# Optimization experiments

Hardware: AMD Instinct MI355X
Metric: run time of the kernel (lower is better)

## Reference

```python
import jax, jax.numpy as jnp
import numpy as np
from math import factorial, comb

N_NODES = 50000
N_EDGES = 640000
FEAT = 32
NUM_BASIS = 8
CUTOFF = 5.0
MAX_Z = 118
NUM_ITERS = 3
LMAX = 2
K = (LMAX + 1) ** 2  # 9 spherical channels for max_degree=2


def _assoc_legendre(c, s, lmax):
    # associated Legendre P_l^m without Condon-Shortley phase
    P = {(0, 0): np.ones_like(c)}
    for m in range(1, lmax + 1):
        P[(m, m)] = P[(m - 1, m - 1)] * (2 * m - 1) * s
    for m in range(lmax):
        P[(m + 1, m)] = (2 * m + 1) * c * P[(m, m)]
    for m in range(lmax + 1):
        for l in range(m + 2, lmax + 1):
            P[(l, m)] = ((2 * l - 1) * c * P[(l - 1, m)] - (l + m - 1) * P[(l - 2, m)]) / (l - m)
    return P


def _real_sh_np(xyz, lmax):
    # Racah-normalized real spherical harmonics (Y_00 = 1), order m=-l..l
    r = np.linalg.norm(xyz, axis=1)
    cth = xyz[:, 2] / r
    sth = np.sqrt(np.maximum(1.0 - cth ** 2, 0.0))
    phi = np.arctan2(xyz[:, 1], xyz[:, 0])
    P = _assoc_legendre(cth, sth, lmax)
    cols = []
    for l in range(lmax + 1):
        for m in range(-l, l + 1):
            am = abs(m)
            if m == 0:
                cols.append(P[(l, 0)])
            else:
                nrm = np.sqrt(2.0 * factorial(l - am) / factorial(l + am))
                ang = np.cos(am * phi) if m > 0 else np.sin(am * phi)
                cols.append(nrm * P[(l, am)] * ang)
    return np.stack(cols, axis=1)


def _gaunt_tensor():
    # cg[k1,k2,k3]: expansion of Y_k1 * Y_k2 onto Y_k3 (degrees <= 2).
    # Products of degree<=2 harmonics lie exactly in span of degree<=4 harmonics,
    # so the least-squares fit below recovers exact coefficients.
    rng = np.random.default_rng(0)
    pts = rng.normal(size=(4096, 3))
    pts /= np.linalg.norm(pts, axis=1, keepdims=True)
    A = _real_sh_np(pts, 2 * LMAX)  # (M, 25)
    Y = A[:, :K]                    # (M, 9)
    prod = (Y[:, :, None] * Y[:, None, :]).reshape(len(pts), K * K)
    coef, *_ = np.linalg.lstsq(A, prod, rcond=None)  # (25, 81)
    return coef[:K].reshape(K, K, K).transpose(1, 2, 0).astype(np.float32)


CG = jnp.asarray(_gaunt_tensor())  # (9, 9, 9)
LOG_BINOM = jnp.asarray([np.log(comb(NUM_BASIS - 1, kk)) for kk in range(NUM_BASIS)], dtype=jnp.float32)


def _sh_l2(u):
    # Racah real SH of unit vectors, degrees 0..2, order m=-l..l
    x, y, z = u[:, 0], u[:, 1], u[:, 2]
    s3 = 1.7320508075688772
    return jnp.stack([
        jnp.ones_like(x),
        y, z, x,
        s3 * x * y, s3 * y * z, 0.5 * (3.0 * z * z - 1.0), s3 * x * z, 0.5 * s3 * (x * x - y * y),
    ], axis=1)


def _radial(r):
    # reciprocal Bernstein basis (log-space, stable) * smooth cutoff
    u = r / (1.0 + r)
    k = jnp.arange(NUM_BASIS, dtype=jnp.float32)
    n = float(NUM_BASIS - 1)
    eps = 1e-12
    logu = jnp.log(jnp.maximum(u, eps))[:, None]
    log1u = jnp.log(jnp.maximum(1.0 - u, eps))[:, None]
    bern = jnp.exp(LOG_BINOM + k * logu + (n - k) * log1u)  # (E, B)
    cut = jnp.where(r < CUTOFF, jnp.exp(-(r * r) / jnp.maximum(CUTOFF * CUTOFF - r * r, eps)), 0.0)
    return bern * cut[:, None]


def _forward(dr_vec, embed, rad_w, d1w, d1b, d2w, d2b, Z, neighbor_idxs):
    idx_i, idx_j = neighbor_idxs[0], neighbor_idxs[1]
    r = jnp.linalg.norm(dr_vec, axis=1)
    u = dr_vec / jnp.maximum(r, 1e-9)[:, None]
    Ysh = _sh_l2(u)              # (E, 9) angular basis
    rad = _radial(r)             # (E, B) radial basis
    # mask padding edges (idx_i == idx_j) as in mask_by_neighbor
    rad = rad * (idx_i != idx_j).astype(rad.dtype)[:, None]

    N = Z.shape[0]
    x = jnp.zeros((N, K, FEAT), jnp.float32).at[:, 0, :].set(embed[Z])

    for i in range(NUM_ITERS):
        last = i == NUM_ITERS - 1
        k3 = 1 if last else K    # last MessagePass has max_degree=0
        xe = x[idx_j]                                  # (E, 9, F) edge gather
        g = jnp.einsum('eb,dbf->edf', rad, rad_w[i])   # (E, 3, F) radial->feature per basis degree
        y = jnp.zeros((N_EDGES, k3, FEAT), jnp.float32)
        for l2 in range(LMAX + 1):
            sl = slice(l2 * l2, (l2 + 1) ** 2)
            c = jnp.einsum('abc,eb->eac', CG[:, sl, :k3], Ysh[:, sl])          # (E, 9, k3)
            y = y + jnp.einsum('eac,eaf->ecf', c, xe * g[:, l2][:, None, :])   # (E, k3, F)
        m = jax.ops.segment_sum(y, idx_i, num_segments=N)                      # scatter-sum
        if last:
            x = x[:, :1, :]      # change_max_degree_or_type(x, 0)
        h = x + m
        h = jnp.einsum('nkf,fg->nkg', h, d1w[i]).at[:, 0, :].add(d1b[i])
        gate = jax.nn.sigmoid(h[:, :1, :])
        h = h * gate             # silu on scalar channel, sigmoid-gated tensor channels
        h = jnp.einsum('nkf,fg->nkg', h, d2w[i]).at[:, 0, :].add(d2b[i])
        x = x + h
    return x[:, 0, :]            # (N, F)


def setup_inputs() -> dict:
    key = jax.random.key(0)
    ks = jax.random.split(key, 8)
    dr_vec = jax.random.normal(ks[0], (N_EDGES, 3), jnp.float32) * 2.0
    Z = jax.random.randint(ks[1], (N_NODES,), 0, MAX_Z + 1, jnp.int32)
    neighbor_idxs = jax.random.randint(ks[2], (2, N_EDGES), 0, N_NODES, jnp.int32)
    embed = jax.random.normal(ks[3], (MAX_Z + 1, FEAT), jnp.float32)
    rad_w = jax.random.normal(ks[4], (NUM_ITERS, LMAX + 1, NUM_BASIS, FEAT), jnp.float32) * 0.5
    d1w = jax.random.normal(ks[5], (NUM_ITERS, FEAT, FEAT), jnp.float32) * (1.0 / np.sqrt(FEAT))
    d1b = jnp.zeros((NUM_ITERS, FEAT), jnp.float32)
    d2w = jax.random.normal(ks[6], (NUM_ITERS, FEAT, FEAT), jnp.float32) * 0.02
    d2b = jnp.zeros((NUM_ITERS, FEAT), jnp.float32)
    return {"dr_vec": dr_vec, "embed": embed, "rad_w": rad_w, "d1w": d1w, "d1b": d1b,
            "d2w": d2w, "d2b": d2b, "Z": Z, "neighbor_idxs": neighbor_idxs}


def reference(dr_vec, embed, rad_w, d1w, d1b, d2w, d2b, Z, neighbor_idxs):
    return _forward(dr_vec, embed, rad_w, d1w, d1b, d2w, d2b, Z, neighbor_idxs)
```

## Files before the change

### kernel.cpp

```cpp
#include <hip/hip_runtime.h>
#include <hip/hip_fp16.h>
#include <math.h>

#define NN 50000
#define NE 640000
#define F  32
#define KCH 9
#define CUT 5.0f

#define C13 (1.0f/3.0f)
#define C23 (2.0f/3.0f)
#define C15 0.2f
#define C25 0.4f
#define C17 (1.0f/7.0f)
#define C27 (2.0f/7.0f)
#define IS3 0.5773502691896258f
#define S35 0.3464101615137755f
#define S37 0.2474358296526968f
#define S3  1.7320508075688772f

union U2H { unsigned int u; __half2 h; };

__device__ __forceinline__ unsigned int pack2(float a, float b) {
    U2H c; c.h = __floats2half2_rn(a, b); return c.u;
}
__device__ __forceinline__ float2 unpack2(unsigned int u) {
    U2H c; c.u = u; return __half22float2(c.h);
}

__global__ __launch_bounds__(256) void init_x(const float* __restrict__ embed,
                                              const int* __restrict__ Z,
                                              float* __restrict__ x,
                                              __half* __restrict__ x0h) {
    int idx = blockIdx.x * 256 + threadIdx.x;
    int n = idx >> 5, f = idx & 31;
    float v = embed[Z[n] * F + f];
    float* xp = x + (size_t)n * KCH * F + f;
    xp[0] = v;
    #pragma unroll
    for (int a = 1; a < KCH; ++a) xp[a * F] = 0.f;
    x0h[idx] = __float2half_rn(v);
}

__global__ __launch_bounds__(256) void hist_kernel(const int* __restrict__ idx_i,
                                                   const int* __restrict__ idx_j,
                                                   const float* __restrict__ dr,
                                                   int* __restrict__ cnt) {
    int e = blockIdx.x * 256 + threadIdx.x;
    if (e >= NE) return;
    int ni = idx_i[e], nj = idx_j[e];
    float dx = dr[3 * e + 0], dy = dr[3 * e + 1], dz = dr[3 * e + 2];
    float r2 = fmaf(dx, dx, fmaf(dy, dy, dz * dz));
    if (ni != nj && r2 < CUT * CUT) atomicAdd(&cnt[ni], 1);
}

#define SCAN_T 1024
#define SCAN_C ((NN + SCAN_T - 1) / SCAN_T)

__global__ __launch_bounds__(SCAN_T) void scan_kernel(const int* __restrict__ cnt,
                                                      int* __restrict__ offs,
                                                      int* __restrict__ head) {
    __shared__ int ps[SCAN_T];
    int t = threadIdx.x;
    int b = t * SCAN_C;
    int e = min(b + SCAN_C, NN);
    int s = 0;
    for (int i = b; i < e; ++i) s += cnt[i];
    ps[t] = s;
    __syncthreads();
    for (int off = 1; off < SCAN_T; off <<= 1) {
        int v = (t >= off) ? ps[t - off] : 0;
        __syncthreads();
        ps[t] += v;
        __syncthreads();
    }
    int run = (t == 0) ? 0 : ps[t - 1];
    for (int i = b; i < e; ++i) { int c = cnt[i]; offs[i] = run; head[i] = run; run += c; }
    if (t == SCAN_T - 1) offs[NN] = ps[SCAN_T - 1];
}

__global__ __launch_bounds__(256) void fill_kernel(const int* __restrict__ idx_i,
                                                   const int* __restrict__ idx_j,
                                                   const float* __restrict__ dr,
                                                   int* __restrict__ head,
                                                   uint2* __restrict__ erec) {
    int e = blockIdx.x * 256 + threadIdx.x;
    if (e >= NE) return;
    int ni = idx_i[e], nj = idx_j[e];
    float dx = dr[3 * e + 0], dy = dr[3 * e + 1], dz = dr[3 * e + 2];
    float r2 = fmaf(dx, dx, fmaf(dy, dy, dz * dz));
    if (!(ni != nj && r2 < CUT * CUT)) return;

    float r = sqrtf(r2);
    float inv = 1.0f / fmaxf(r, 1e-9f);
    float ux = dx * inv, uy = dy * inv, uz = dz * inv;

    float cut = expf(-r2 / fmaxf(CUT * CUT - r2, 1e-12f));
    float ur = r / (1.0f + r), vr = 1.0f - ur;
    float up2 = ur*ur, up3 = up2*ur, up4 = up3*ur, up5 = up4*ur, up6 = up5*ur, up7 = up6*ur;
    float vp2 = vr*vr, vp3 = vp2*vr, vp4 = vp3*vr, vp5 = vp4*vr, vp6 = vp5*vr, vp7 = vp6*vr;

    float rc0 = cut * vp7;
    float rc1 = cut * 7.f  * ur  * vp6;
    float rc2 = cut * 21.f * up2 * vp5;
    float rc3 = cut * 35.f * up3 * vp4;
    float rc4 = cut * 35.f * up4 * vp3;
    float rc5 = cut * 21.f * up5 * vp2;
    float rc6 = cut * 7.f  * up6 * vr;
    float rc7 = cut * up7;

    int p = atomicAdd(&head[ni], 1);
    uint2 e0, e1, e2;
    U2H zh; zh.h = __floats2half2_rn(uz, 0.f);
    e0.x = pack2(ux, uy);
    e0.y = (zh.u & 0xFFFFu) | ((unsigned int)nj << 16);
    e1.x = pack2(rc0, rc1); e1.y = pack2(rc2, rc3);
    e2.x = pack2(rc4, rc5); e2.y = pack2(rc6, rc7);
    erec[(size_t)3 * p + 0] = e0;
    erec[(size_t)3 * p + 1] = e1;
    erec[(size_t)3 * p + 2] = e2;
}

template<int MODE>
__global__ __launch_bounds__(256) void gather_kernel(const uint2* __restrict__ erec,
                                                     const __half* __restrict__ x0h,
                                                     const uint4* __restrict__ xhA,
                                                     const ushort* __restrict__ xhB,
                                                     const float* __restrict__ rw_iter,
                                                     const int* __restrict__ offs,
                                                     float* __restrict__ m) {
    const int NWAVES = 2048 * 4;
    int lane = threadIdx.x & 63;
    int wid  = threadIdx.x >> 6;
    int half = lane >> 5;
    int f    = lane & 31;
    int gw   = blockIdx.x * 4 + wid;

    float rwv[24];
    #pragma unroll
    for (int lb = 0; lb < 24; ++lb) rwv[lb] = rw_iter[lb * F + f];
    if (MODE == 2) {
        #pragma unroll
        for (int lb = 8; lb < 16; ++lb) rwv[lb] *= C13;
        #pragma unroll
        for (int lb = 16; lb < 24; ++lb) rwv[lb] *= C15;
    }

    constexpr int NACC = (MODE == 2) ? 1 : KCH;

    for (int n = gw; n < NN; n += NWAVES) {
        int start = offs[n], end = offs[n + 1];

        float acc[NACC];
        #pragma unroll
        for (int a = 0; a < NACC; ++a) acc[a] = 0.f;

        int t = start + half;
        uint2 e0_c = {}, e0_n = {};
        uint4 xa_c = {};
        ushort x8_c = 0;

        if (t < end) {
            e0_c = erec[(size_t)3 * t + 0];
            int nj0 = (int)(e0_c.y >> 16);
            if (MODE == 0) {
                x8_c = __half_as_ushort(x0h[nj0 * F + f]);
            } else {
                xa_c = xhA[nj0 * F + f];
                x8_c = xhB[nj0 * F + f];
            }
            int t2 = (t + 2 < end) ? t + 2 : t;
            e0_n = erec[(size_t)3 * t2 + 0];
        }

        while (t < end) {
            int tn = t + 2;
            int tnc = (tn < end) ? tn : t;
            int tfc = (tn + 2 < end) ? tn + 2 : tnc;

            int njn = (int)(e0_n.y >> 16);
            uint4 xa_n = {};
            ushort x8_n;
            if (MODE == 0) {
                x8_n = __half_as_ushort(x0h[njn * F + f]);
            } else {
                xa_n = xhA[njn * F + f];
                x8_n = xhB[njn * F + f];
            }
            uint2 e0_f = erec[(size_t)3 * tfc + 0];

            uint2 e1 = erec[(size_t)3 * t + 1];
            uint2 e2 = erec[(size_t)3 * t + 2];

            float2 uxy = unpack2(e0_c.x);
            float ux = uxy.x, uy = uxy.y;
            float uz = unpack2(e0_c.y).x;
            float2 rcA = unpack2(e1.x);
            float2 rcB = unpack2(e1.y);
            float2 rcC = unpack2(e2.x);
            float2 rcD = unpack2(e2.y);

            float g0, g1, g2;
            g0 = rcA.x * rwv[0];
            g0 = fmaf(rcA.y, rwv[1], g0); g0 = fmaf(rcB.x, rwv[2], g0); g0 = fmaf(rcB.y, rwv[3], g0);
            g0 = fmaf(rcC.x, rwv[4], g0); g0 = fmaf(rcC.y, rwv[5], g0); g0 = fmaf(rcD.x, rwv[6], g0);
            g0 = fmaf(rcD.y, rwv[7], g0);
            g1 = rcA.x * rwv[8];
            g1 = fmaf(rcA.y, rwv[9],  g1); g1 = fmaf(rcB.x, rwv[10], g1); g1 = fmaf(rcB.y, rwv[11], g1);
            g1 = fmaf(rcC.x, rwv[12], g1); g1 = fmaf(rcC.y, rwv[13], g1); g1 = fmaf(rcD.x, rwv[14], g1);
            g1 = fmaf(rcD.y, rwv[15], g1);
            g2 = rcA.x * rwv[16];
            g2 = fmaf(rcA.y, rwv[17], g2); g2 = fmaf(rcB.x, rwv[18], g2); g2 = fmaf(rcB.y, rwv[19], g2);
            g2 = fmaf(rcC.x, rwv[20], g2); g2 = fmaf(rcC.y, rwv[21], g2); g2 = fmaf(rcD.x, rwv[22], g2);
            g2 = fmaf(rcD.y, rwv[23], g2);

            if (MODE == 0) {
                float xe0 = __half2float(__ushort_as_half(x8_c));
                float s2 = S3 * g2;
                acc[0] = fmaf(xe0, g0, acc[0]);
                acc[1] = fmaf(xe0, uy * g1, acc[1]);
                acc[2] = fmaf(xe0, uz * g1, acc[2]);
                acc[3] = fmaf(xe0, ux * g1, acc[3]);
                acc[4] = fmaf(xe0, s2 * ux * uy, acc[4]);
                acc[5] = fmaf(xe0, s2 * uy * uz, acc[5]);
                acc[6] = fmaf(xe0, fmaf(1.5f * uz, uz, -0.5f) * g2, acc[6]);
                acc[7] = fmaf(xe0, s2 * ux * uz, acc[7]);
                acc[8] = fmaf(xe0, 0.5f * s2 * (ux * ux - uy * uy), acc[8]);
            } else {
                float xe[9];
                {
                    float2 p;
                    p = unpack2(xa_c.x); xe[0] = p.x; xe[1] = p.y;
                    p = unpack2(xa_c.y); xe[2] = p.x; xe[3] = p.y;
                    p = unpack2(xa_c.z); xe[4] = p.x; xe[5] = p.y;
                    p = unpack2(xa_c.w); xe[6] = p.x; xe[7] = p.y;
                    xe[8] = __half2float(__ushort_as_half(x8_c));
                }
                if (MODE == 2) {
                    float dot1 = uy * xe[1];
                    dot1 = fmaf(uz, xe[2], dot1);
                    dot1 = fmaf(ux, xe[3], dot1);
                    float Y4 = S3 * ux * uy, Y5 = S3 * uy * uz, Y7 = S3 * ux * uz;
                    float Y6 = fmaf(1.5f * uz, uz, -0.5f);
                    float Y8 = 0.5f * S3 * (ux * ux - uy * uy);
                    float dot2 = Y4 * xe[4];
                    dot2 = fmaf(Y5, xe[5], dot2);
                    dot2 = fmaf(Y6, xe[6], dot2);
                    dot2 = fmaf(Y7, xe[7], dot2);
                    dot2 = fmaf(Y8, xe[8], dot2);
                    acc[0] = fmaf(g0, xe[0], acc[0]);
                    acc[0] = fmaf(g1, dot1, acc[0]);
                    acc[0] = fmaf(g2, dot2, acc[0]);
                } else {
                    float s2 = S3 * g2;
                    float w[9];
                    w[0] = g0;
                    w[1] = uy * g1; w[2] = uz * g1; w[3] = ux * g1;
                    w[4] = s2 * ux * uy;
                    w[5] = s2 * uy * uz;
                    w[6] = fmaf(1.5f * uz, uz, -0.5f) * g2;
                    w[7] = s2 * ux * uz;
                    w[8] = 0.5f * s2 * (ux * ux - uy * uy);

                    float d0 = xe[0]*w[0], d1 = xe[1]*w[1], d2 = xe[2]*w[2], d3 = xe[3]*w[3];
                    float d4 = xe[4]*w[4], d5 = xe[5]*w[5], d6 = xe[6]*w[6], d7 = xe[7]*w[7];
                    float d8 = xe[8]*w[8];

                    acc[0] += d0 + C13 * (d1 + d2 + d3) + C15 * (d4 + d5 + d6 + d7 + d8);
                    #define T(a, b) (xe[a] * w[b] + xe[b] * w[a])
                    acc[1] += T(0,1) - C15 * T(1,6) - S35 * T(1,8) + S35 * T(2,5) + S35 * T(3,4);
                    acc[2] += T(0,2) + S35 * T(1,5) + C25 * T(2,6) + S35 * T(3,7);
                    acc[3] += T(0,3) + S35 * T(1,4) + S35 * T(2,7) - C15 * T(3,6) + S35 * T(3,8);
                    acc[4] += T(0,4) + IS3 * T(1,3) - C27 * T(4,6) + S37 * T(5,7);
                    acc[5] += T(0,5) + IS3 * T(1,2) + S37 * T(4,7) + C17 * T(5,6) - S37 * T(5,8);
                    acc[6] += T(0,6) - C13 * d1 + C23 * d2 - C13 * d3
                            - C27 * d4 + C17 * d5 + C27 * d6 + C17 * d7 - C27 * d8;
                    acc[7] += T(0,7) + IS3 * T(2,3) + S37 * T(4,5) + C17 * T(6,7) + S37 * T(7,8);
                    acc[8] += T(0,8) - IS3 * d1 + IS3 * d3 - S37 * d5 + S37 * d7 - C27 * T(6,8);
                    #undef T
                }
            }

            e0_c = e0_n; e0_n = e0_f;
            xa_c = xa_n; x8_c = x8_n;
            t = tn;
        }

        #pragma unroll
        for (int a = 0; a < NACC; ++a) acc[a] += __shfl_xor(acc[a], 32);

        if (half == 0) {
            if (MODE == 2) {
                m[(size_t)n * F + f] = acc[0];
            } else {
                float* mp = m + (size_t)n * KCH * F + f;
                #pragma unroll
                for (int a = 0; a < KCH; ++a) mp[a * F] = acc[a];
            }
        }
    }
}

__global__ __launch_bounds__(256) void node_full(float* __restrict__ x,
                                                 const float* __restrict__ m,
                                                 uint4* __restrict__ xhA,
                                                 ushort* __restrict__ xhB,
                                                 const float* __restrict__ w1,
                                                 const float* __restrict__ b1,
                                                 const float* __restrict__ w2,
                                                 const float* __restrict__ b2) {
    __shared__ float tile[8][KCH][F];
    int nl = threadIdx.x >> 5, f = threadIdx.x & 31;
    int n = blockIdx.x * 8 + nl;

    float w1c[F];
    #pragma unroll
    for (int fi = 0; fi < F; ++fi) w1c[fi] = w1[fi * F + f];

    float xk[KCH];
    #pragma unroll
    for (int k = 0; k < KCH; ++k) {
        xk[k] = x[((size_t)n * KCH + k) * F + f];
        tile[nl][k][f] = xk[k] + m[((size_t)n * KCH + k) * F + f];
    }
    __syncthreads();

    float o1[KCH];
    #pragma unroll
    for (int k = 0; k < KCH; ++k) {
        float s = 0.f;
        #pragma unroll
        for (int fi = 0; fi < F; ++fi) s = fmaf(tile[nl][k][fi], w1c[fi], s);
        o1[k] = s;
    }
    o1[0] += b1[f];
    float gate = 1.0f / (1.0f + expf(-o1[0]));
    __syncthreads();
    #pragma unroll
    for (int k = 0; k < KCH; ++k) tile[nl][k][f] = o1[k] * gate;
    __syncthreads();

    float w2c[F];
    #pragma unroll
    for (int fi = 0; fi < F; ++fi) w2c[fi] = w2[fi * F + f];

    float xn[KCH];
    #pragma unroll
    for (int k = 0; k < KCH; ++k) {
        float s = (k == 0) ? b2[f] : 0.f;
        #pragma unroll
        for (int fi = 0; fi < F; ++fi) s = fmaf(tile[nl][k][fi], w2c[fi], s);
        xn[k] = xk[k] + s;
        x[((size_t)n * KCH + k) * F + f] = xn[k];
    }

    uint4 ua;
    ua.x = pack2(xn[0], xn[1]); ua.y = pack2(xn[2], xn[3]);
    ua.z = pack2(xn[4], xn[5]); ua.w = pack2(xn[6], xn[7]);
    xhA[n * F + f] = ua;
    xhB[n * F + f] = __half_as_ushort(__float2half_rn(xn[8]));
}

__global__ __launch_bounds__(256) void node_last(const float* __restrict__ x,
                                                 const float* __restrict__ m1,
                                                 const float* __restrict__ w1,
                                                 const float* __restrict__ b1,
                                                 const float* __restrict__ w2,
                                                 const float* __restrict__ b2,
                                                 float* __restrict__ out) {
    __shared__ float tile[8][F];
    int nl = threadIdx.x >> 5, f = threadIdx.x & 31;
    int n = blockIdx.x * 8 + nl;

    float w1c[F];
    #pragma unroll
    for (int fi = 0; fi < F; ++fi) w1c[fi] = w1[fi * F + f];

    float x0 = x[(size_t)n * KCH * F + f];
    tile[nl][f] = x0 + m1[(size_t)n * F + f];
    __syncthreads();
    float s = 0.f;
    #pragma unroll
    for (int fi = 0; fi < F; ++fi) s = fmaf(tile[nl][fi], w1c[fi], s);
    s += b1[f];
    float gate = 1.0f / (1.0f + expf(-s));
    float h2 = s * gate;
    __syncthreads();
    tile[nl][f] = h2;
    __syncthreads();
    float w2c[F];
    #pragma unroll
    for (int fi = 0; fi < F; ++fi) w2c[fi] = w2[fi * F + f];
    float o = b2[f];
    #pragma unroll
    for (int fi = 0; fi < F; ++fi) o = fmaf(tile[nl][fi], w2c[fi], o);
    out[(size_t)n * F + f] = x0 + o;
}

extern "C" void kernel_launch(void* const* d_in, const int* in_sizes, int n_in,
                              void* d_out, int out_size, void* d_ws, size_t ws_size,
                              hipStream_t stream) {
    (void)in_sizes; (void)n_in; (void)out_size; (void)ws_size;
    const float* dr    = (const float*)d_in[0];
    const float* embed = (const float*)d_in[1];
    const float* rad_w = (const float*)d_in[2];
    const float* d1w   = (const float*)d_in[3];
    const float* d1b   = (const float*)d_in[4];
    const float* d2w   = (const float*)d_in[5];
    const float* d2b   = (const float*)d_in[6];
    const int*   Z     = (const int*)d_in[7];
    const int*   nidx  = (const int*)d_in[8];
    const int* idx_i = nidx;
    const int* idx_j = nidx + NE;

    float* x   = (float*)d_ws;
    float* m   = x + (size_t)NN * KCH * F;
    uint4* xhA = (uint4*)(m + (size_t)NN * KCH * F);
    __half* x0h = (__half*)(xhA + (size_t)NN * F);
    ushort* xhB = (ushort*)(x0h + (size_t)NN * F);
    uint2* erec = (uint2*)(xhB + (size_t)NN * F);
    int* offs = (int*)(erec + (size_t)3 * NE);
    int* head = offs + (NN + 1);
    int* cnt  = head + NN;
    float* outp = (float*)d_out;

    hipMemsetAsync(cnt, 0, NN * sizeof(int), stream);
    hist_kernel<<<(NE + 255) / 256, 256, 0, stream>>>(idx_i, idx_j, dr, cnt);
    scan_kernel<<<1, SCAN_T, 0, stream>>>(cnt, offs, head);
    fill_kernel<<<(NE + 255) / 256, 256, 0, stream>>>(idx_i, idx_j, dr, head, erec);

    init_x<<<NN * F / 256, 256, 0, stream>>>(embed, Z, x, x0h);

    for (int i = 0; i < 3; ++i) {
        const float* rwi = rad_w + (size_t)i * 3 * 8 * F;
        const float* w1 = d1w + (size_t)i * F * F;
        const float* b1 = d1b + (size_t)i * F;
        const float* w2 = d2w + (size_t)i * F * F;
        const float* b2 = d2b + (size_t)i * F;
        if (i == 0) {
            gather_kernel<0><<<2048, 256, 0, stream>>>(erec, x0h, xhA, xhB, rwi, offs, m);
            node_full<<<NN / 8, 256, 0, stream>>>(x, m, xhA, xhB, w1, b1, w2, b2);
        } else if (i == 1) {
            gather_kernel<1><<<2048, 256, 0, stream>>>(erec, x0h, xhA, xhB, rwi, offs, m);
            node_full<<<NN / 8, 256, 0, stream>>>(x, m, xhA, xhB, w1, b1, w2, b2);
        } else {
            gather_kernel<2><<<2048, 256, 0, stream>>>(erec, x0h, xhA, xhB, rwi, offs, m);
            node_last<<<NN / 8, 256, 0, stream>>>(x, m, w1, b1, w2, b2, outp);
        }
    }
}
```

Measured before the change: 583.5 us.

## Drop fp32 node state for fp16 copies and deepen gather prefetch

The full fp32 9-channel node state is replaced by the existing fp16 packed copies, with only channel 0 kept in fp32. node_full now reads channels 1-8 from the half buffers and writes back only x0 plus the packed halves, which cuts node-kernel traffic. The gather loop's software pipeline goes from one to two edges of lookahead on neighbor loads, to hide more gather latency. Higher channels now round-trip through fp16 between iterations, which can add error, and the deeper prefetch uses more registers.

```diff
diff --git a/kernel.cpp b/kernel.cpp
--- a/kernel.cpp
+++ b/kernel.cpp
@@ -27,19 +27,25 @@
 __device__ __forceinline__ float2 unpack2(unsigned int u) {
     U2H c; c.u = u; return __half22float2(c.h);
 }
+__device__ __forceinline__ float h2f(ushort u) {
+    return __half2float(__ushort_as_half(u));
+}
 
 __global__ __launch_bounds__(256) void init_x(const float* __restrict__ embed,
                                               const int* __restrict__ Z,
-                                              float* __restrict__ x,
-                                              __half* __restrict__ x0h) {
+                                              float* __restrict__ x0,
+                                              ushort* __restrict__ x0h,
+                                              uint4* __restrict__ xhA,
+                                              ushort* __restrict__ xhB) {
     int idx = blockIdx.x * 256 + threadIdx.x;
     int n = idx >> 5, f = idx & 31;
     float v = embed[Z[n] * F + f];
-    float* xp = x + (size_t)n * KCH * F + f;
-    xp[0] = v;
-    #pragma unroll
-    for (int a = 1; a < KCH; ++a) xp[a * F] = 0.f;
-    x0h[idx] = __float2half_rn(v);
+    x0[idx] = v;
+    unsigned int p = pack2(v, 0.f);
+    x0h[idx] = (ushort)(p & 0xFFFFu);
+    uint4 ua; ua.x = p; ua.y = 0u; ua.z = 0u; ua.w = 0u;
+    xhA[idx] = ua;
+    xhB[idx] = 0;
 }
 
 __global__ __launch_bounds__(256) void hist_kernel(const int* __restrict__ idx_i,
@@ -123,7 +129,7 @@
 
 template<int MODE>
 __global__ __launch_bounds__(256) void gather_kernel(const uint2* __restrict__ erec,
-                                                     const __half* __restrict__ x0h,
+                                                     const ushort* __restrict__ x0h,
                                                      const uint4* __restrict__ xhA,
                                                      const ushort* __restrict__ xhB,
                                                      const float* __restrict__ rw_iter,
@@ -156,45 +162,46 @@
         for (int a = 0; a < NACC; ++a) acc[a] = 0.f;
 
         int t = start + half;
-        uint2 e0_c = {}, e0_n = {};
-        uint4 xa_c = {};
-        ushort x8_c = 0;
+        uint2 e0_0 = {}, e0_1 = {}, e0_2 = {};
+        uint4 xa_0 = {}, xa_1 = {};
+        ushort x8_0 = 0, x8_1 = 0;
 
         if (t < end) {
-            e0_c = erec[(size_t)3 * t + 0];
-            int nj0 = (int)(e0_c.y >> 16);
+            int c1 = min(t + 2, end - 1);
+            int c2 = min(t + 4, end - 1);
+            e0_0 = erec[(size_t)3 * t];
+            e0_1 = erec[(size_t)3 * c1];
+            e0_2 = erec[(size_t)3 * c2];
+            int nj0 = (int)(e0_0.y >> 16);
+            int nj1 = (int)(e0_1.y >> 16);
             if (MODE == 0) {
-                x8_c = __half_as_ushort(x0h[nj0 * F + f]);
+                x8_0 = x0h[nj0 * F + f];
+                x8_1 = x0h[nj1 * F + f];
             } else {
-                xa_c = xhA[nj0 * F + f];
-                x8_c = xhB[nj0 * F + f];
+                xa_0 = xhA[nj0 * F + f]; x8_0 = xhB[nj0 * F + f];
+                xa_1 = xhA[nj1 * F + f]; x8_1 = xhB[nj1 * F + f];
             }
-            int t2 = (t + 2 < end) ? t + 2 : t;
-            e0_n = erec[(size_t)3 * t2 + 0];
         }
 
         while (t < end) {
-            int tn = t + 2;
-            int tnc = (tn < end) ? tn : t;
-            int tfc = (tn + 2 < end) ? tn + 2 : tnc;
-
-            int njn = (int)(e0_n.y >> 16);
-            uint4 xa_n = {};
-            ushort x8_n;
-            if (MODE == 0) {
-                x8_n = __half_as_ushort(x0h[njn * F + f]);
-            } else {
-                xa_n = xhA[njn * F + f];
-                x8_n = xhB[njn * F + f];
-            }
-            uint2 e0_f = erec[(size_t)3 * tfc + 0];
-
             uint2 e1 = erec[(size_t)3 * t + 1];
             uint2 e2 = erec[(size_t)3 * t + 2];
 
-            float2 uxy = unpack2(e0_c.x);
+            int c3 = min(t + 6, end - 1);
+            uint2 e0_3 = erec[(size_t)3 * c3];
+            int nj2 = (int)(e0_2.y >> 16);
+            uint4 xa_2 = {};
+            ushort x8_2;
+            if (MODE == 0) {
+                x8_2 = x0h[nj2 * F + f];
+            } else {
+                xa_2 = xhA[nj2 * F + f];
+                x8_2 = xhB[nj2 * F + f];
+            }
+
+            float2 uxy = unpack2(e0_0.x);
             float ux = uxy.x, uy = uxy.y;
-            float uz = unpack2(e0_c.y).x;
+            float uz = unpack2(e0_0.y).x;
             float2 rcA = unpack2(e1.x);
             float2 rcB = unpack2(e1.y);
             float2 rcC = unpack2(e2.x);
@@ -215,7 +222,7 @@
             g2 = fmaf(rcD.y, rwv[23], g2);
 
             if (MODE == 0) {
-                float xe0 = __half2float(__ushort_as_half(x8_c));
+                float xe0 = h2f(x8_0);
                 float s2 = S3 * g2;
                 acc[0] = fmaf(xe0, g0, acc[0]);
                 acc[1] = fmaf(xe0, uy * g1, acc[1]);
@@ -230,11 +237,11 @@
                 float xe[9];
                 {
                     float2 p;
-                    p = unpack2(xa_c.x); xe[0] = p.x; xe[1] = p.y;
-                    p = unpack2(xa_c.y); xe[2] = p.x; xe[3] = p.y;
-                    p = unpack2(xa_c.z); xe[4] = p.x; xe[5] = p.y;
-                    p = unpack2(xa_c.w); xe[6] = p.x; xe[7] = p.y;
-                    xe[8] = __half2float(__ushort_as_half(x8_c));
+                    p = unpack2(xa_0.x); xe[0] = p.x; xe[1] = p.y;
+                    p = unpack2(xa_0.y); xe[2] = p.x; xe[3] = p.y;
+                    p = unpack2(xa_0.z); xe[4] = p.x; xe[5] = p.y;
+                    p = unpack2(xa_0.w); xe[6] = p.x; xe[7] = p.y;
+                    xe[8] = h2f(x8_0);
                 }
                 if (MODE == 2) {
                     float dot1 = uy * xe[1];
@@ -281,9 +288,10 @@
                 }
             }
 
-            e0_c = e0_n; e0_n = e0_f;
-            xa_c = xa_n; x8_c = x8_n;
-            t = tn;
+            e0_0 = e0_1; e0_1 = e0_2; e0_2 = e0_3;
+            xa_0 = xa_1; xa_1 = xa_2;
+            x8_0 = x8_1; x8_1 = x8_2;
+            t += 2;
         }
 
         #pragma unroll
@@ -301,7 +309,7 @@
     }
 }
 
-__global__ __launch_bounds__(256) void node_full(float* __restrict__ x,
+__global__ __launch_bounds__(256) void node_full(float* __restrict__ x0,
                                                  const float* __restrict__ m,
                                                  uint4* __restrict__ xhA,
                                                  ushort* __restrict__ xhB,
@@ -318,11 +326,21 @@
     for (int fi = 0; fi < F; ++fi) w1c[fi] = w1[fi * F + f];
 
     float xk[KCH];
-    #pragma unroll
-    for (int k = 0; k < KCH; ++k) {
-        xk[k] = x[((size_t)n * KCH + k) * F + f];
+    {
+        uint4 ua = xhA[n * F + f];
+        ushort ub = xhB[n * F + f];
+        float2 p;
+        p = unpack2(ua.x); xk[0] = p.x; xk[1] = p.y;
+        p = unpack2(ua.y); xk[2] = p.x; xk[3] = p.y;
+        p = unpack2(ua.z); xk[4] = p.x; xk[5] = p.y;
+        p = unpack2(ua.w); xk[6] = p.x; xk[7] = p.y;
+        xk[8] = h2f(ub);
+    }
+    xk[0] = x0[n * F + f];
+
+    #pragma unroll
+    for (int k = 0; k < KCH; ++k)
         tile[nl][k][f] = xk[k] + m[((size_t)n * KCH + k) * F + f];
-    }
     __syncthreads();
 
     float o1[KCH];
@@ -351,9 +369,9 @@
         #pragma unroll
         for (int fi = 0; fi < F; ++fi) s = fmaf(tile[nl][k][fi], w2c[fi], s);
         xn[k] = xk[k] + s;
-        x[((size_t)n * KCH + k) * F + f] = xn[k];
-    }
-
+    }
+
+    x0[n * F + f] = xn[0];
     uint4 ua;
     ua.x = pack2(xn[0], xn[1]); ua.y = pack2(xn[2], xn[3]);
     ua.z = pack2(xn[4], xn[5]); ua.w = pack2(xn[6], xn[7]);
@@ -361,7 +379,7 @@
     xhB[n * F + f] = __half_as_ushort(__float2half_rn(xn[8]));
 }
 
-__global__ __launch_bounds__(256) void node_last(const float* __restrict__ x,
+__global__ __launch_bounds__(256) void node_last(const float* __restrict__ x0,
                                                  const float* __restrict__ m1,
                                                  const float* __restrict__ w1,
                                                  const float* __restrict__ b1,
@@ -376,8 +394,8 @@
     #pragma unroll
     for (int fi = 0; fi < F; ++fi) w1c[fi] = w1[fi * F + f];
 
-    float x0 = x[(size_t)n * KCH * F + f];
-    tile[nl][f] = x0 + m1[(size_t)n * F + f];
+    float xv = x0[n * F + f];
+    tile[nl][f] = xv + m1[(size_t)n * F + f];
     __syncthreads();
     float s = 0.f;
     #pragma unroll
@@ -394,7 +412,7 @@
     float o = b2[f];
     #pragma unroll
     for (int fi = 0; fi < F; ++fi) o = fmaf(tile[nl][fi], w2c[fi], o);
-    out[(size_t)n * F + f] = x0 + o;
+    out[(size_t)n * F + f] = xv + o;
 }
 
 extern "C" void kernel_launch(void* const* d_in, const int* in_sizes, int n_in,
@@ -413,11 +431,11 @@
     const int* idx_i = nidx;
     const int* idx_j = nidx + NE;
 
-    float* x   = (float*)d_ws;
-    float* m   = x + (size_t)NN * KCH * F;
-    uint4* xhA = (uint4*)(m + (size_t)NN * KCH * F);
-    __half* x0h = (__half*)(xhA + (size_t)NN * F);
-    ushort* xhB = (ushort*)(x0h + (size_t)NN * F);
+    uint4* xhA = (uint4*)d_ws;
+    float* m   = (float*)(xhA + (size_t)NN * F);
+    float* x0  = m + (size_t)NN * KCH * F;
+    ushort* x0h = (ushort*)(x0 + (size_t)NN * F);
+    ushort* xhB = x0h + (size_t)NN * F;
     uint2* erec = (uint2*)(xhB + (size_t)NN * F);
     int* offs = (int*)(erec + (size_t)3 * NE);
     int* head = offs + (NN + 1);
@@ -429,7 +447,7 @@
     scan_kernel<<<1, SCAN_T, 0, stream>>>(cnt, offs, head);
     fill_kernel<<<(NE + 255) / 256, 256, 0, stream>>>(idx_i, idx_j, dr, head, erec);
 
-    init_x<<<NN * F / 256, 256, 0, stream>>>(embed, Z, x, x0h);
+    init_x<<<NN * F / 256, 256, 0, stream>>>(embed, Z, x0, x0h, xhA, xhB);
 
     for (int i = 0; i < 3; ++i) {
         const float* rwi = rad_w + (size_t)i * 3 * 8 * F;
@@ -439,13 +457,13 @@
         const float* b2 = d2b + (size_t)i * F;
         if (i == 0) {
             gather_kernel<0><<<2048, 256, 0, stream>>>(erec, x0h, xhA, xhB, rwi, offs, m);
-            node_full<<<NN / 8, 256, 0, stream>>>(x, m, xhA, xhB, w1, b1, w2, b2);
+            node_full<<<NN / 8, 256, 0, stream>>>(x0, m, xhA, xhB, w1, b1, w2, b2);
         } else if (i == 1) {
             gather_kernel<1><<<2048, 256, 0, stream>>>(erec, x0h, xhA, xhB, rwi, offs, m);
-            node_full<<<NN / 8, 256, 0, stream>>>(x, m, xhA, xhB, w1, b1, w2, b2);
+            node_full<<<NN / 8, 256, 0, stream>>>(x0, m, xhA, xhB, w1, b1, w2, b2);
         } else {
             gather_kernel<2><<<2048, 256, 0, stream>>>(erec, x0h, xhA, xhB, rwi, offs, m);
-            node_last<<<NN / 8, 256, 0, stream>>>(x, m, w1, b1, w2, b2, outp);
+            node_last<<<NN / 8, 256, 0, stream>>>(x0, m, w1, b1, w2, b2, outp);
         }
     }
 }
```

Result: faster. 571.2 us (-2.1%).
